# Performance work log

Hardware: AMD Instinct MI355X
Metric: run time of the kernel (lower is better)

The kernel has to match this reference:

```python
import jax, jax.numpy as jnp
import numpy as np

N_EXPERTS = 8
EMB = 1024
HID = 2816


def setup_inputs() -> dict:
    key = jax.random.key(0)
    k1, k2, k3, k4, k5 = jax.random.split(key, 5)
    x = jax.random.normal(k1, (2, 2048, EMB), dtype=jnp.float32)
    w_router = jax.random.normal(k2, (EMB, N_EXPERTS), dtype=jnp.float32) * 0.02
    w1 = jax.random.normal(k3, (N_EXPERTS, EMB, HID), dtype=jnp.float32) * 0.02
    w3 = jax.random.normal(k4, (N_EXPERTS, EMB, HID), dtype=jnp.float32) * 0.02
    w2 = jax.random.normal(k5, (N_EXPERTS, HID, EMB), dtype=jnp.float32) * 0.02
    return {"x": x, "w_router": w_router, "w1": w1, "w3": w3, "w2": w2,
            "n_experts_per_token": 2}


def reference(x, w_router, w1, w3, w2, n_experts_per_token):
    # x: (b, s, d) -> flatten to tokens (t, d)
    orig_shape = x.shape
    xf = x.reshape(-1, orig_shape[-1])                      # (t, d)
    scores = xf @ w_router                                  # (t, E)
    top_v, top_i = jax.lax.top_k(scores, n_experts_per_token)  # (t, k)
    top_p = jax.nn.softmax(top_v, axis=-1)                  # (t, k)
    # dense per-token gate over experts (top-k indices are distinct)
    gates = jnp.sum(jax.nn.one_hot(top_i, w_router.shape[-1], dtype=x.dtype)
                    * top_p[..., None], axis=1)             # (t, E)
    # SwiGLU for every expert (dense reference for the masked dispatch)
    h = jnp.einsum('td,edh->teh', xf, w1)                   # (t, E, H)
    g = jnp.einsum('td,edh->teh', xf, w3)                   # (t, E, H)
    expert_out = jnp.einsum('teh,ehd->ted', jax.nn.silu(h) * g, w2)  # (t, E, d)
    y = jnp.einsum('ted,te->td', expert_out, gates)
    return y.reshape(orig_shape)
```

## Files before the change

### kernel.cpp

```cpp
#include <hip/hip_runtime.h>
#include <hip/hip_bf16.h>

#define N_EXPERTS 8
#define EMB 1024
#define HID 2816
#define NTOK 4096
#define NSLOT (NTOK * 2)
#define TLIST NTOK

typedef float f32x4 __attribute__((ext_vector_type(4)));
typedef short short8 __attribute__((ext_vector_type(8)));

static __device__ __forceinline__ unsigned short f2bf(float v) {
    __hip_bfloat16 b = __float2bfloat16(v);
    return *reinterpret_cast<unsigned short*>(&b);
}

static __device__ __forceinline__ void ldst16(const unsigned short* g, unsigned short* l) {
    __builtin_amdgcn_global_load_lds(
        (const __attribute__((address_space(1))) unsigned int*)g,
        (__attribute__((address_space(3))) unsigned int*)l,
        16, 0, 0);
}

__global__ __launch_bounds__(256) void transpose_cvt_all(const float* __restrict__ w1,
                                                         const float* __restrict__ w3,
                                                         const float* __restrict__ w2,
                                                         unsigned short* __restrict__ w1T,
                                                         unsigned short* __restrict__ w3T,
                                                         unsigned short* __restrict__ w2T) {
    __shared__ unsigned short tile[64][68];
    int z = blockIdx.z;
    int which = z >> 3, e = z & 7;
    const float* in;
    unsigned short* out;
    int R, C, r0, c0;
    if (which == 0)      { in = w1; out = w1T; R = EMB; C = HID; r0 = blockIdx.y * 64; c0 = blockIdx.x * 64; }
    else if (which == 1) { in = w3; out = w3T; R = EMB; C = HID; r0 = blockIdx.y * 64; c0 = blockIdx.x * 64; }
    else                 { in = w2; out = w2T; R = HID; C = EMB; r0 = blockIdx.x * 64; c0 = blockIdx.y * 64; }
    const float* src = in + (size_t)e * R * C;
    unsigned short* dst = out + (size_t)e * R * C;
    int tid = threadIdx.x;
#pragma unroll
    for (int i = 0; i < 4; ++i) {
        int lin = i * 256 + tid;
        int r = lin >> 4, c4 = (lin & 15) * 4;
        float4 v = *(const float4*)&src[(size_t)(r0 + r) * C + c0 + c4];
        ushort4 b;
        b.x = f2bf(v.x); b.y = f2bf(v.y); b.z = f2bf(v.z); b.w = f2bf(v.w);
        *(ushort4*)&tile[r][c4] = b;
    }
    __syncthreads();
#pragma unroll
    for (int i = 0; i < 4; ++i) {
        int lin = i * 256 + tid;
        int c = lin >> 4, r4 = (lin & 15) * 4;
        ushort4 b;
        b.x = tile[r4 + 0][c]; b.y = tile[r4 + 1][c];
        b.z = tile[r4 + 2][c]; b.w = tile[r4 + 3][c];
        *(ushort4*)&dst[(size_t)(c0 + c) * R + r0 + r4] = b;
    }
}

__global__ __launch_bounds__(256) void zero_out(float* __restrict__ p) {
    int gid = blockIdx.x * 256 + threadIdx.x;
    float4 z = {0.f, 0.f, 0.f, 0.f};
    ((float4*)p)[gid] = z;
}

__global__ __launch_bounds__(64) void router_kernel(const float* __restrict__ x,
                                                    const float* __restrict__ wr,
                                                    unsigned short* __restrict__ xbf,
                                                    int* __restrict__ sel,
                                                    float* __restrict__ gates) {
    int t = blockIdx.x, lane = threadIdx.x;
    const float* xr = x + (size_t)t * EMB;
    float acc[N_EXPERTS];
#pragma unroll
    for (int e = 0; e < N_EXPERTS; ++e) acc[e] = 0.f;
    for (int d = lane; d < EMB; d += 64) {
        float xv = xr[d];
        xbf[(size_t)t * EMB + d] = f2bf(xv);
        const float* w = wr + d * N_EXPERTS;
#pragma unroll
        for (int e = 0; e < N_EXPERTS; ++e) acc[e] += xv * w[e];
    }
#pragma unroll
    for (int off = 32; off; off >>= 1) {
#pragma unroll
        for (int e = 0; e < N_EXPERTS; ++e) acc[e] += __shfl_xor(acc[e], off, 64);
    }
    if (lane == 0) {
        int b0 = 0; float v0 = acc[0];
#pragma unroll
        for (int e = 1; e < N_EXPERTS; ++e) if (acc[e] > v0) { v0 = acc[e]; b0 = e; }
        int b1 = -1; float v1 = -1e30f;
#pragma unroll
        for (int e = 0; e < N_EXPERTS; ++e) if (e != b0 && acc[e] > v1) { v1 = acc[e]; b1 = e; }
        float g0 = 1.f / (1.f + expf(v1 - v0));
        float g1 = 1.f - g0;
        sel[t] = b0 | (b1 << 8);
        gates[2 * t] = g0;
        gates[2 * t + 1] = g1;
    }
}

__global__ __launch_bounds__(256) void build_lists(const int* __restrict__ sel,
                                                   int* __restrict__ counts,
                                                   int* __restrict__ lists) {
    int e = blockIdx.x;
    int tid = threadIdx.x, lane = tid & 63, wid = tid >> 6;
    __shared__ int wsum[4];
    __shared__ int running;
    if (tid == 0) running = 0;
    __syncthreads();
    for (int base = 0; base < NTOK; base += 256) {
        int tok = base + tid;
        int s = sel[tok];
        int e0 = s & 0xff, e1 = (s >> 8) & 0xff;
        bool take = (e0 == e) || (e1 == e);
        int slot = (e0 == e) ? 2 * tok : 2 * tok + 1;
        unsigned long long b = __ballot(take);
        int lp = __popcll(b & ((1ull << lane) - 1ull));
        if (lane == 0) wsum[wid] = __popcll(b);
        __syncthreads();
        int off = running;
        for (int w = 0; w < wid; ++w) off += wsum[w];
        if (take) lists[e * TLIST + off + lp] = slot;
        __syncthreads();
        if (tid == 0) running += wsum[0] + wsum[1] + wsum[2] + wsum[3];
        __syncthreads();
    }
    if (tid == 0) counts[e] = running;
}

__global__ __launch_bounds__(256) void gemm1_kernel(const unsigned short* __restrict__ xbf,
                                                    const unsigned short* __restrict__ w1T,
                                                    const unsigned short* __restrict__ w3T,
                                                    unsigned short* __restrict__ h,
                                                    const int* __restrict__ counts,
                                                    const int* __restrict__ lists) {
    int e = blockIdx.z;
    int cnt = counts[e];
    int rt = blockIdx.y;
    if (rt * 128 >= cnt) return;
    int n0 = blockIdx.x * 64;

    __shared__ unsigned short As[128 * 32];
    __shared__ unsigned short B1s[64 * 32];
    __shared__ unsigned short B3s[64 * 32];
    __shared__ int slotArr[128];

    int tid = threadIdx.x;
    if (tid < 128) {
        int r = rt * 128 + tid;
        slotArr[tid] = (r < cnt) ? lists[e * TLIST + r] : -1;
    }
    __syncthreads();

    int lane = tid & 63, wid = tid >> 6;
    int seg = lane >> 2, chunk = lane & 3;

    int rA0 = wid * 32 + seg, rA1 = wid * 32 + 16 + seg;
    int s0 = slotArr[rA0], s1 = slotArr[rA1];
    int t0 = s0 >= 0 ? (s0 >> 1) : 0, t1 = s1 >= 0 ? (s1 >> 1) : 0;
    const unsigned short* gA0 = xbf + (size_t)t0 * EMB + chunk * 8;
    const unsigned short* gA1 = xbf + (size_t)t1 * EMB + chunk * 8;
    int rB = n0 + wid * 16 + seg;
    const unsigned short* gB1 = w1T + ((size_t)e * HID + rB) * EMB + chunk * 8;
    const unsigned short* gB3 = w3T + ((size_t)e * HID + rB) * EMB + chunk * 8;
    unsigned short* lA0 = &As[wid * 1024];
    unsigned short* lA1 = &As[wid * 1024 + 512];
    unsigned short* lB1 = &B1s[wid * 512];
    unsigned short* lB3 = &B3s[wid * 512];

    int wr = wid >> 1, wc = wid & 1;
    int lrow = lane & 15, quad = lane >> 4;

    f32x4 zero4 = {0.f, 0.f, 0.f, 0.f};
    f32x4 acc1[4][2], acc3[4][2];
#pragma unroll
    for (int mt = 0; mt < 4; ++mt)
#pragma unroll
        for (int nt = 0; nt < 2; ++nt) { acc1[mt][nt] = zero4; acc3[mt][nt] = zero4; }

    const int KT = EMB / 32;
    for (int kt = 0; kt < KT; ++kt) {
        ldst16(gA0, lA0); ldst16(gA1, lA1);
        ldst16(gB1, lB1); ldst16(gB3, lB3);
        gA0 += 32; gA1 += 32; gB1 += 32; gB3 += 32;
        __builtin_amdgcn_s_waitcnt(0);
        __syncthreads();
        short8 af[4], b1f[2], b3f[2];
#pragma unroll
        for (int mt = 0; mt < 4; ++mt)
            af[mt] = *(const short8*)&As[(wr * 64 + mt * 16 + lrow) * 32 + quad * 8];
#pragma unroll
        for (int nt = 0; nt < 2; ++nt) {
            b1f[nt] = *(const short8*)&B1s[(wc * 32 + nt * 16 + lrow) * 32 + quad * 8];
            b3f[nt] = *(const short8*)&B3s[(wc * 32 + nt * 16 + lrow) * 32 + quad * 8];
        }
#pragma unroll
        for (int mt = 0; mt < 4; ++mt)
#pragma unroll
            for (int nt = 0; nt < 2; ++nt) {
                acc1[mt][nt] = __builtin_amdgcn_mfma_f32_16x16x32_bf16(af[mt], b1f[nt], acc1[mt][nt], 0, 0, 0);
                acc3[mt][nt] = __builtin_amdgcn_mfma_f32_16x16x32_bf16(af[mt], b3f[nt], acc3[mt][nt], 0, 0, 0);
            }
        __syncthreads();
    }

#pragma unroll
    for (int mt = 0; mt < 4; ++mt) {
#pragma unroll
        for (int i = 0; i < 4; ++i) {
            int r = wr * 64 + mt * 16 + quad * 4 + i;
            int slot = slotArr[r];
            if (slot < 0) continue;
#pragma unroll
            for (int nt = 0; nt < 2; ++nt) {
                float v1 = acc1[mt][nt][i];
                float v3 = acc3[mt][nt][i];
                float hv = v1 / (1.f + __expf(-v1)) * v3;
                int c = n0 + wc * 32 + nt * 16 + lrow;
                h[(size_t)slot * HID + c] = f2bf(hv);
            }
        }
    }
}

__global__ __launch_bounds__(256) void gemm2_kernel(const unsigned short* __restrict__ h,
                                                    const unsigned short* __restrict__ w2T,
                                                    float* __restrict__ out,
                                                    const int* __restrict__ counts,
                                                    const int* __restrict__ lists,
                                                    const float* __restrict__ gates) {
    int e = blockIdx.z;
    int cnt = counts[e];
    int rt = blockIdx.y;
    if (rt * 128 >= cnt) return;
    int n0 = blockIdx.x * 128;

    __shared__ unsigned short As[128 * 32];
    __shared__ unsigned short Bs[128 * 32];
    __shared__ int slotArr[128];

    int tid = threadIdx.x;
    if (tid < 128) {
        int r = rt * 128 + tid;
        slotArr[tid] = (r < cnt) ? lists[e * TLIST + r] : -1;
    }
    __syncthreads();

    int lane = tid & 63, wid = tid >> 6;
    int seg = lane >> 2, chunk = lane & 3;

    int rA0 = wid * 32 + seg, rA1 = wid * 32 + 16 + seg;
    int s0 = slotArr[rA0], s1 = slotArr[rA1];
    const unsigned short* gA0 = h + (size_t)(s0 < 0 ? 0 : s0) * HID + chunk * 8;
    const unsigned short* gA1 = h + (size_t)(s1 < 0 ? 0 : s1) * HID + chunk * 8;
    int rB0 = n0 + wid * 32 + seg, rB1 = rB0 + 16;
    const unsigned short* gB0 = w2T + ((size_t)e * EMB + rB0) * HID + chunk * 8;
    const unsigned short* gB1 = w2T + ((size_t)e * EMB + rB1) * HID + chunk * 8;
    unsigned short* lA0 = &As[wid * 1024];
    unsigned short* lA1 = &As[wid * 1024 + 512];
    unsigned short* lB0 = &Bs[wid * 1024];
    unsigned short* lB1 = &Bs[wid * 1024 + 512];

    int wr = wid >> 1, wc = wid & 1;
    int lrow = lane & 15, quad = lane >> 4;

    f32x4 zero4 = {0.f, 0.f, 0.f, 0.f};
    f32x4 acc[4][4];
#pragma unroll
    for (int mt = 0; mt < 4; ++mt)
#pragma unroll
        for (int nt = 0; nt < 4; ++nt) acc[mt][nt] = zero4;

    const int KT = HID / 32;
    for (int kt = 0; kt < KT; ++kt) {
        ldst16(gA0, lA0); ldst16(gA1, lA1);
        ldst16(gB0, lB0); ldst16(gB1, lB1);
        gA0 += 32; gA1 += 32; gB0 += 32; gB1 += 32;
        __builtin_amdgcn_s_waitcnt(0);
        __syncthreads();
        short8 af[4], bf[4];
#pragma unroll
        for (int mt = 0; mt < 4; ++mt)
            af[mt] = *(const short8*)&As[(wr * 64 + mt * 16 + lrow) * 32 + quad * 8];
#pragma unroll
        for (int nt = 0; nt < 4; ++nt)
            bf[nt] = *(const short8*)&Bs[(wc * 64 + nt * 16 + lrow) * 32 + quad * 8];
#pragma unroll
        for (int mt = 0; mt < 4; ++mt)
#pragma unroll
            for (int nt = 0; nt < 4; ++nt)
                acc[mt][nt] = __builtin_amdgcn_mfma_f32_16x16x32_bf16(af[mt], bf[nt], acc[mt][nt], 0, 0, 0);
        __syncthreads();
    }

#pragma unroll
    for (int mt = 0; mt < 4; ++mt) {
#pragma unroll
        for (int i = 0; i < 4; ++i) {
            int r = wr * 64 + mt * 16 + quad * 4 + i;
            int slot = slotArr[r];
            if (slot < 0) continue;
            float g = gates[slot];
            int tok = slot >> 1;
#pragma unroll
            for (int nt = 0; nt < 4; ++nt) {
                int c = n0 + wc * 64 + nt * 16 + lrow;
                atomicAdd(&out[(size_t)tok * EMB + c], g * acc[mt][nt][i]);
            }
        }
    }
}

extern "C" void kernel_launch(void* const* d_in, const int* in_sizes, int n_in,
                              void* d_out, int out_size, void* d_ws, size_t ws_size,
                              hipStream_t stream) {
    const float* x = (const float*)d_in[0];
    const float* wrout = (const float*)d_in[1];
    const float* w1 = (const float*)d_in[2];
    const float* w3 = (const float*)d_in[3];
    const float* w2 = (const float*)d_in[4];
    float* out = (float*)d_out;

    char* ws = (char*)d_ws;
    const size_t SW = (size_t)N_EXPERTS * EMB * HID * 2;
    const size_t SX = (size_t)NTOK * EMB * 2;
    const size_t SH = (size_t)NSLOT * HID * 2;
    const size_t SMETA = 256 + (size_t)N_EXPERTS * TLIST * 4 + (size_t)NSLOT * 4 + (size_t)NTOK * 4;
    const size_t NEEDED = 3 * SW + SX + SH + SMETA;
    if (ws_size < NEEDED) return;

    unsigned short* w1T = (unsigned short*)(ws);
    unsigned short* w3T = (unsigned short*)(ws + SW);
    unsigned short* w2T = (unsigned short*)(ws + 2 * SW);
    unsigned short* xbf = (unsigned short*)(ws + 3 * SW);
    unsigned short* hbuf = (unsigned short*)(ws + 3 * SW + SX);
    char* meta = ws + 3 * SW + SX + SH;
    int* counts = (int*)meta;
    int* lists = (int*)(meta + 256);
    float* gates = (float*)(meta + 256 + (size_t)N_EXPERTS * TLIST * 4);
    int* sel = (int*)(meta + 256 + (size_t)N_EXPERTS * TLIST * 4 + (size_t)NSLOT * 4);

    transpose_cvt_all<<<dim3(HID / 64, EMB / 64, 3 * N_EXPERTS), 256, 0, stream>>>(
        w1, w3, w2, w1T, w3T, w2T);

    zero_out<<<NTOK * EMB / 4 / 256, 256, 0, stream>>>(out);

    router_kernel<<<NTOK, 64, 0, stream>>>(x, wrout, xbf, sel, gates);
    build_lists<<<N_EXPERTS, 256, 0, stream>>>(sel, counts, lists);

    gemm1_kernel<<<dim3(HID / 64, NTOK / 128, N_EXPERTS), 256, 0, stream>>>(
        xbf, w1T, w3T, hbuf, counts, lists);
    gemm2_kernel<<<dim3(EMB / 128, NTOK / 128, N_EXPERTS), 256, 0, stream>>>(
        hbuf, w2T, out, counts, lists, gates);
}
```

Baseline: 552.3 us.

## Double K-tile depth with XOR-swizzled LDS and fold output zeroing into router

Both expert GEMMs now stage a 64-wide K slice per iteration instead of 32, which halves the number of barrier and wait rounds per tile. An XOR swizzle on the LDS column chunks avoids bank conflicts when the wider rows are read. The separate zero_out kernel is removed and the router zeroes the output rows while it vectorizes its loads of x and the router weights. The cost is doubled shared memory per block, which may lower occupancy.

```diff
diff --git a/kernel.cpp b/kernel.cpp
--- a/kernel.cpp
+++ b/kernel.cpp
@@ -62,28 +62,38 @@
     }
 }
 
-__global__ __launch_bounds__(256) void zero_out(float* __restrict__ p) {
-    int gid = blockIdx.x * 256 + threadIdx.x;
-    float4 z = {0.f, 0.f, 0.f, 0.f};
-    ((float4*)p)[gid] = z;
-}
-
 __global__ __launch_bounds__(64) void router_kernel(const float* __restrict__ x,
                                                     const float* __restrict__ wr,
                                                     unsigned short* __restrict__ xbf,
                                                     int* __restrict__ sel,
-                                                    float* __restrict__ gates) {
+                                                    float* __restrict__ gates,
+                                                    float* __restrict__ out) {
     int t = blockIdx.x, lane = threadIdx.x;
     const float* xr = x + (size_t)t * EMB;
+    float* outr = out + (size_t)t * EMB;
     float acc[N_EXPERTS];
 #pragma unroll
     for (int e = 0; e < N_EXPERTS; ++e) acc[e] = 0.f;
-    for (int d = lane; d < EMB; d += 64) {
-        float xv = xr[d];
-        xbf[(size_t)t * EMB + d] = f2bf(xv);
-        const float* w = wr + d * N_EXPERTS;
-#pragma unroll
-        for (int e = 0; e < N_EXPERTS; ++e) acc[e] += xv * w[e];
+    const float4 z4 = {0.f, 0.f, 0.f, 0.f};
+#pragma unroll
+    for (int i = 0; i < 4; ++i) {
+        int d = i * 256 + lane * 4;
+        float4 v = *(const float4*)&xr[d];
+        ushort4 b;
+        b.x = f2bf(v.x); b.y = f2bf(v.y); b.z = f2bf(v.z); b.w = f2bf(v.w);
+        *(ushort4*)&xbf[(size_t)t * EMB + d] = b;
+        float vv[4] = {v.x, v.y, v.z, v.w};
+#pragma unroll
+        for (int j = 0; j < 4; ++j) {
+            const float* w = wr + (size_t)(d + j) * N_EXPERTS;
+            float4 wa = *(const float4*)&w[0];
+            float4 wb = *(const float4*)&w[4];
+            acc[0] += vv[j] * wa.x; acc[1] += vv[j] * wa.y;
+            acc[2] += vv[j] * wa.z; acc[3] += vv[j] * wa.w;
+            acc[4] += vv[j] * wb.x; acc[5] += vv[j] * wb.y;
+            acc[6] += vv[j] * wb.z; acc[7] += vv[j] * wb.w;
+        }
+        *(float4*)&outr[d] = z4;
     }
 #pragma unroll
     for (int off = 32; off; off >>= 1) {
@@ -146,9 +156,9 @@
     if (rt * 128 >= cnt) return;
     int n0 = blockIdx.x * 64;
 
-    __shared__ unsigned short As[128 * 32];
-    __shared__ unsigned short B1s[64 * 32];
-    __shared__ unsigned short B3s[64 * 32];
+    __shared__ unsigned short As[128 * 64];
+    __shared__ unsigned short B1s[64 * 64];
+    __shared__ unsigned short B3s[64 * 64];
     __shared__ int slotArr[128];
 
     int tid = threadIdx.x;
@@ -159,23 +169,34 @@
     __syncthreads();
 
     int lane = tid & 63, wid = tid >> 6;
-    int seg = lane >> 2, chunk = lane & 3;
-
-    int rA0 = wid * 32 + seg, rA1 = wid * 32 + 16 + seg;
-    int s0 = slotArr[rA0], s1 = slotArr[rA1];
-    int t0 = s0 >= 0 ? (s0 >> 1) : 0, t1 = s1 >= 0 ? (s1 >> 1) : 0;
-    const unsigned short* gA0 = xbf + (size_t)t0 * EMB + chunk * 8;
-    const unsigned short* gA1 = xbf + (size_t)t1 * EMB + chunk * 8;
-    int rB = n0 + wid * 16 + seg;
-    const unsigned short* gB1 = w1T + ((size_t)e * HID + rB) * EMB + chunk * 8;
-    const unsigned short* gB3 = w3T + ((size_t)e * HID + rB) * EMB + chunk * 8;
-    unsigned short* lA0 = &As[wid * 1024];
-    unsigned short* lA1 = &As[wid * 1024 + 512];
-    unsigned short* lB1 = &B1s[wid * 512];
-    unsigned short* lB3 = &B3s[wid * 512];
+    int lr8 = lane >> 3;
+    int kswz = ((lane & 7) ^ lr8) * 8;
+
+    int ra0 = wid * 32 + 0 * 8 + lr8, ra1 = wid * 32 + 1 * 8 + lr8;
+    int ra2 = wid * 32 + 2 * 8 + lr8, ra3 = wid * 32 + 3 * 8 + lr8;
+    int sa0 = slotArr[ra0], sa1 = slotArr[ra1], sa2 = slotArr[ra2], sa3 = slotArr[ra3];
+    const unsigned short* gA0 = xbf + (size_t)(sa0 >= 0 ? (sa0 >> 1) : 0) * EMB + kswz;
+    const unsigned short* gA1 = xbf + (size_t)(sa1 >= 0 ? (sa1 >> 1) : 0) * EMB + kswz;
+    const unsigned short* gA2 = xbf + (size_t)(sa2 >= 0 ? (sa2 >> 1) : 0) * EMB + kswz;
+    const unsigned short* gA3 = xbf + (size_t)(sa3 >= 0 ? (sa3 >> 1) : 0) * EMB + kswz;
+    int rb0 = n0 + wid * 16 + 0 * 8 + lr8, rb1 = n0 + wid * 16 + 1 * 8 + lr8;
+    const unsigned short* gB1_0 = w1T + ((size_t)e * HID + rb0) * EMB + kswz;
+    const unsigned short* gB1_1 = w1T + ((size_t)e * HID + rb1) * EMB + kswz;
+    const unsigned short* gB3_0 = w3T + ((size_t)e * HID + rb0) * EMB + kswz;
+    const unsigned short* gB3_1 = w3T + ((size_t)e * HID + rb1) * EMB + kswz;
+
+    unsigned short* lA0 = &As[(wid * 32 + 0) * 64];
+    unsigned short* lA1 = &As[(wid * 32 + 8) * 64];
+    unsigned short* lA2 = &As[(wid * 32 + 16) * 64];
+    unsigned short* lA3 = &As[(wid * 32 + 24) * 64];
+    unsigned short* lB1_0 = &B1s[(wid * 16 + 0) * 64];
+    unsigned short* lB1_1 = &B1s[(wid * 16 + 8) * 64];
+    unsigned short* lB3_0 = &B3s[(wid * 16 + 0) * 64];
+    unsigned short* lB3_1 = &B3s[(wid * 16 + 8) * 64];
 
     int wr = wid >> 1, wc = wid & 1;
     int lrow = lane & 15, quad = lane >> 4;
+    int rsw = lrow & 7;
 
     f32x4 zero4 = {0.f, 0.f, 0.f, 0.f};
     f32x4 acc1[4][2], acc3[4][2];
@@ -184,29 +205,37 @@
 #pragma unroll
         for (int nt = 0; nt < 2; ++nt) { acc1[mt][nt] = zero4; acc3[mt][nt] = zero4; }
 
-    const int KT = EMB / 32;
+    const int KT = EMB / 64;
     for (int kt = 0; kt < KT; ++kt) {
-        ldst16(gA0, lA0); ldst16(gA1, lA1);
-        ldst16(gB1, lB1); ldst16(gB3, lB3);
-        gA0 += 32; gA1 += 32; gB1 += 32; gB3 += 32;
+        ldst16(gA0, lA0); ldst16(gA1, lA1); ldst16(gA2, lA2); ldst16(gA3, lA3);
+        ldst16(gB1_0, lB1_0); ldst16(gB1_1, lB1_1);
+        ldst16(gB3_0, lB3_0); ldst16(gB3_1, lB3_1);
+        gA0 += 64; gA1 += 64; gA2 += 64; gA3 += 64;
+        gB1_0 += 64; gB1_1 += 64; gB3_0 += 64; gB3_1 += 64;
         __builtin_amdgcn_s_waitcnt(0);
         __syncthreads();
-        short8 af[4], b1f[2], b3f[2];
-#pragma unroll
-        for (int mt = 0; mt < 4; ++mt)
-            af[mt] = *(const short8*)&As[(wr * 64 + mt * 16 + lrow) * 32 + quad * 8];
-#pragma unroll
-        for (int nt = 0; nt < 2; ++nt) {
-            b1f[nt] = *(const short8*)&B1s[(wc * 32 + nt * 16 + lrow) * 32 + quad * 8];
-            b3f[nt] = *(const short8*)&B3s[(wc * 32 + nt * 16 + lrow) * 32 + quad * 8];
+#pragma unroll
+        for (int ks = 0; ks < 2; ++ks) {
+            short8 af[4], b1f[2], b3f[2];
+#pragma unroll
+            for (int mt = 0; mt < 4; ++mt)
+                af[mt] = *(const short8*)&As[(wr * 64 + mt * 16 + lrow) * 64 +
+                                             (((ks * 4 + quad) ^ rsw) * 8)];
+#pragma unroll
+            for (int nt = 0; nt < 2; ++nt) {
+                b1f[nt] = *(const short8*)&B1s[(wc * 32 + nt * 16 + lrow) * 64 +
+                                               (((ks * 4 + quad) ^ rsw) * 8)];
+                b3f[nt] = *(const short8*)&B3s[(wc * 32 + nt * 16 + lrow) * 64 +
+                                               (((ks * 4 + quad) ^ rsw) * 8)];
+            }
+#pragma unroll
+            for (int mt = 0; mt < 4; ++mt)
+#pragma unroll
+                for (int nt = 0; nt < 2; ++nt) {
+                    acc1[mt][nt] = __builtin_amdgcn_mfma_f32_16x16x32_bf16(af[mt], b1f[nt], acc1[mt][nt], 0, 0, 0);
+                    acc3[mt][nt] = __builtin_amdgcn_mfma_f32_16x16x32_bf16(af[mt], b3f[nt], acc3[mt][nt], 0, 0, 0);
+                }
         }
-#pragma unroll
-        for (int mt = 0; mt < 4; ++mt)
-#pragma unroll
-            for (int nt = 0; nt < 2; ++nt) {
-                acc1[mt][nt] = __builtin_amdgcn_mfma_f32_16x16x32_bf16(af[mt], b1f[nt], acc1[mt][nt], 0, 0, 0);
-                acc3[mt][nt] = __builtin_amdgcn_mfma_f32_16x16x32_bf16(af[mt], b3f[nt], acc3[mt][nt], 0, 0, 0);
-            }
         __syncthreads();
     }
 
@@ -241,8 +270,8 @@
     if (rt * 128 >= cnt) return;
     int n0 = blockIdx.x * 128;
 
-    __shared__ unsigned short As[128 * 32];
-    __shared__ unsigned short Bs[128 * 32];
+    __shared__ unsigned short As[128 * 64];
+    __shared__ unsigned short Bs[128 * 64];
     __shared__ int slotArr[128];
 
     int tid = threadIdx.x;
@@ -253,22 +282,35 @@
     __syncthreads();
 
     int lane = tid & 63, wid = tid >> 6;
-    int seg = lane >> 2, chunk = lane & 3;
-
-    int rA0 = wid * 32 + seg, rA1 = wid * 32 + 16 + seg;
-    int s0 = slotArr[rA0], s1 = slotArr[rA1];
-    const unsigned short* gA0 = h + (size_t)(s0 < 0 ? 0 : s0) * HID + chunk * 8;
-    const unsigned short* gA1 = h + (size_t)(s1 < 0 ? 0 : s1) * HID + chunk * 8;
-    int rB0 = n0 + wid * 32 + seg, rB1 = rB0 + 16;
-    const unsigned short* gB0 = w2T + ((size_t)e * EMB + rB0) * HID + chunk * 8;
-    const unsigned short* gB1 = w2T + ((size_t)e * EMB + rB1) * HID + chunk * 8;
-    unsigned short* lA0 = &As[wid * 1024];
-    unsigned short* lA1 = &As[wid * 1024 + 512];
-    unsigned short* lB0 = &Bs[wid * 1024];
-    unsigned short* lB1 = &Bs[wid * 1024 + 512];
+    int lr8 = lane >> 3;
+    int kswz = ((lane & 7) ^ lr8) * 8;
+
+    int ra0 = wid * 32 + 0 * 8 + lr8, ra1 = wid * 32 + 1 * 8 + lr8;
+    int ra2 = wid * 32 + 2 * 8 + lr8, ra3 = wid * 32 + 3 * 8 + lr8;
+    int sa0 = slotArr[ra0], sa1 = slotArr[ra1], sa2 = slotArr[ra2], sa3 = slotArr[ra3];
+    const unsigned short* gA0 = h + (size_t)(sa0 >= 0 ? sa0 : 0) * HID + kswz;
+    const unsigned short* gA1 = h + (size_t)(sa1 >= 0 ? sa1 : 0) * HID + kswz;
+    const unsigned short* gA2 = h + (size_t)(sa2 >= 0 ? sa2 : 0) * HID + kswz;
+    const unsigned short* gA3 = h + (size_t)(sa3 >= 0 ? sa3 : 0) * HID + kswz;
+    int rb0 = n0 + wid * 32 + 0 * 8 + lr8, rb1 = n0 + wid * 32 + 1 * 8 + lr8;
+    int rb2 = n0 + wid * 32 + 2 * 8 + lr8, rb3 = n0 + wid * 32 + 3 * 8 + lr8;
+    const unsigned short* gB0 = w2T + ((size_t)e * EMB + rb0) * HID + kswz;
+    const unsigned short* gB1 = w2T + ((size_t)e * EMB + rb1) * HID + kswz;
+    const unsigned short* gB2 = w2T + ((size_t)e * EMB + rb2) * HID + kswz;
+    const unsigned short* gB3 = w2T + ((size_t)e * EMB + rb3) * HID + kswz;
+
+    unsigned short* lA0 = &As[(wid * 32 + 0) * 64];
+    unsigned short* lA1 = &As[(wid * 32 + 8) * 64];
+    unsigned short* lA2 = &As[(wid * 32 + 16) * 64];
+    unsigned short* lA3 = &As[(wid * 32 + 24) * 64];
+    unsigned short* lB0 = &Bs[(wid * 32 + 0) * 64];
+    unsigned short* lB1 = &Bs[(wid * 32 + 8) * 64];
+    unsigned short* lB2 = &Bs[(wid * 32 + 16) * 64];
+    unsigned short* lB3 = &Bs[(wid * 32 + 24) * 64];
 
     int wr = wid >> 1, wc = wid & 1;
     int lrow = lane & 15, quad = lane >> 4;
+    int rsw = lrow & 7;
 
     f32x4 zero4 = {0.f, 0.f, 0.f, 0.f};
     f32x4 acc[4][4];
@@ -277,25 +319,31 @@
 #pragma unroll
         for (int nt = 0; nt < 4; ++nt) acc[mt][nt] = zero4;
 
-    const int KT = HID / 32;
+    const int KT = HID / 64;
     for (int kt = 0; kt < KT; ++kt) {
-        ldst16(gA0, lA0); ldst16(gA1, lA1);
-        ldst16(gB0, lB0); ldst16(gB1, lB1);
-        gA0 += 32; gA1 += 32; gB0 += 32; gB1 += 32;
+        ldst16(gA0, lA0); ldst16(gA1, lA1); ldst16(gA2, lA2); ldst16(gA3, lA3);
+        ldst16(gB0, lB0); ldst16(gB1, lB1); ldst16(gB2, lB2); ldst16(gB3, lB3);
+        gA0 += 64; gA1 += 64; gA2 += 64; gA3 += 64;
+        gB0 += 64; gB1 += 64; gB2 += 64; gB3 += 64;
         __builtin_amdgcn_s_waitcnt(0);
         __syncthreads();
-        short8 af[4], bf[4];
-#pragma unroll
-        for (int mt = 0; mt < 4; ++mt)
-            af[mt] = *(const short8*)&As[(wr * 64 + mt * 16 + lrow) * 32 + quad * 8];
-#pragma unroll
-        for (int nt = 0; nt < 4; ++nt)
-            bf[nt] = *(const short8*)&Bs[(wc * 64 + nt * 16 + lrow) * 32 + quad * 8];
-#pragma unroll
-        for (int mt = 0; mt < 4; ++mt)
+#pragma unroll
+        for (int ks = 0; ks < 2; ++ks) {
+            short8 af[4], bf[4];
+#pragma unroll
+            for (int mt = 0; mt < 4; ++mt)
+                af[mt] = *(const short8*)&As[(wr * 64 + mt * 16 + lrow) * 64 +
+                                             (((ks * 4 + quad) ^ rsw) * 8)];
 #pragma unroll
             for (int nt = 0; nt < 4; ++nt)
-                acc[mt][nt] = __builtin_amdgcn_mfma_f32_16x16x32_bf16(af[mt], bf[nt], acc[mt][nt], 0, 0, 0);
+                bf[nt] = *(const short8*)&Bs[(wc * 64 + nt * 16 + lrow) * 64 +
+                                             (((ks * 4 + quad) ^ rsw) * 8)];
+#pragma unroll
+            for (int mt = 0; mt < 4; ++mt)
+#pragma unroll
+                for (int nt = 0; nt < 4; ++nt)
+                    acc[mt][nt] = __builtin_amdgcn_mfma_f32_16x16x32_bf16(af[mt], bf[nt], acc[mt][nt], 0, 0, 0);
+        }
         __syncthreads();
     }
 
@@ -349,9 +397,7 @@
     transpose_cvt_all<<<dim3(HID / 64, EMB / 64, 3 * N_EXPERTS), 256, 0, stream>>>(
         w1, w3, w2, w1T, w3T, w2T);
 
-    zero_out<<<NTOK * EMB / 4 / 256, 256, 0, stream>>>(out);
-
-    router_kernel<<<NTOK, 64, 0, stream>>>(x, wrout, xbf, sel, gates);
+    router_kernel<<<NTOK, 64, 0, stream>>>(x, wrout, xbf, sel, gates, out);
     build_lists<<<N_EXPERTS, 256, 0, stream>>>(sel, counts, lists);
 
     gemm1_kernel<<<dim3(HID / 64, NTOK / 128, N_EXPERTS), 256, 0, stream>>>(
```

Measured after the change: 576.9 us. +4.5%, slower.
